# Kernel optimization log

Hardware: AMD Instinct MI355X
Metric: run time of the kernel (lower is better)

The kernel has to match this reference:

```python
import jax, jax.numpy as jnp
import numpy as np

B, LQ, LKV = 4, 2048, 2048
E, AUG, H = 2048, 1024, 16
DH = E // H
EPS = 1e-6


def setup_inputs() -> dict:
    key = jax.random.key(0)
    ks = jax.random.split(key, 6)
    s = lambda d: 1.0 / np.sqrt(d)
    return {
        "query": jax.random.normal(ks[0], (B, LQ, E), jnp.float32),
        "aug_hidden_state": jax.random.normal(ks[1], (B, LKV, AUG), jnp.float32),
        "aug_mask": jnp.ones((B, LKV), jnp.float32),
        "proj_w": jax.random.normal(ks[2], (E, AUG), jnp.float32) * s(AUG),
        "proj_b": jnp.zeros((E,), jnp.float32),
        "in_proj_w": jax.random.normal(ks[3], (3 * E, E), jnp.float32) * s(E),
        "in_proj_b": jnp.zeros((3 * E,), jnp.float32),
        "out_proj_w": jax.random.normal(ks[4], (E, E), jnp.float32) * s(E),
        "out_proj_b": jnp.zeros((E,), jnp.float32),
        "rms_w": jnp.zeros((E,), jnp.float32),
    }


def reference(query, aug_hidden_state, aug_mask, proj_w, proj_b,
              in_proj_w, in_proj_b, out_proj_w, out_proj_b, rms_w):
    del aug_mask  # asserted but never used by the original forward
    # key and value: two identical Linear calls in the original -> same tensor
    kv = aug_hidden_state @ proj_w.T + proj_b                      # [B,LKV,E]
    wq, wk, wv = jnp.split(in_proj_w, 3, axis=0)
    bq, bk, bv = jnp.split(in_proj_b, 3, axis=0)
    q = (query @ wq.T + bq).reshape(B, LQ, H, DH)
    k = (kv @ wk.T + bk).reshape(B, LKV, H, DH)
    v = (kv @ wv.T + bv).reshape(B, LKV, H, DH)
    scale = 1.0 / np.sqrt(DH)
    scores = jnp.einsum("bqhd,bkhd->bhqk", q * scale, k)           # [B,H,LQ,LKV]
    attn = jax.nn.softmax(scores, axis=-1)
    ctx = jnp.einsum("bhqk,bkhd->bqhd", attn, v).reshape(B, LQ, E)
    attn_out = ctx @ out_proj_w.T + out_proj_b                      # [B,LQ,E]
    # GemmaRMSNorm: fp32 norm, (1 + weight) gain
    x32 = attn_out.astype(jnp.float32)
    normed = x32 * jax.lax.rsqrt(jnp.mean(x32 * x32, axis=-1, keepdims=True) + EPS)
    attn_out = (normed * (1.0 + rms_w)).astype(attn_out.dtype)
    return attn_out + query
```

## Files before the change

kernel.cpp:

```cpp
#include <hip/hip_runtime.h>
#include <hip/hip_bf16.h>
#include <stdint.h>

#define B_   4
#define LQ_  2048
#define LKV_ 2048
#define E_   2048
#define AUG_ 1024
#define H_   16
#define DH_  128

typedef unsigned short u16;
typedef __bf16 bf16x8 __attribute__((ext_vector_type(8)));
typedef float f32x4 __attribute__((ext_vector_type(4)));
typedef float f32x16 __attribute__((ext_vector_type(16)));
typedef int i32x2 __attribute__((ext_vector_type(2)));

__device__ __forceinline__ u16 f2bf(float f) {
  union { float f; unsigned u; } v; v.f = f;
  unsigned r = v.u + 0x7fffu + ((v.u >> 16) & 1u);
  return (u16)(r >> 16);
}
__device__ __forceinline__ unsigned pk2(float a, float b) {
  return (unsigned)f2bf(a) | ((unsigned)f2bf(b) << 16);
}
__device__ __forceinline__ float bf2f(u16 u) {
  union { unsigned u; float f; } v; v.u = (unsigned)u << 16; return v.f;
}
__device__ __forceinline__ unsigned cvtpk_bf16(float lo, float hi) {
  unsigned r;
  asm("v_cvt_pk_bf16_f32 %0, %1, %2" : "=v"(r) : "v"(lo), "v"(hi));
  return r;
}
__device__ __forceinline__ float fast_ex2(float x) {
  float r;
  asm("v_exp_f32 %0, %1" : "=v"(r) : "v"(x));
  return r;
}

#define GLDS(gsrc, ldst)                                                        \
  __builtin_amdgcn_global_load_lds(                                             \
      (__attribute__((address_space(1))) void*)(uintptr_t)(gsrc),               \
      (__attribute__((address_space(3))) void*)(unsigned)(uintptr_t)(ldst),     \
      16, 0, 0)

#define BARRIER()                                   \
  do {                                              \
    asm volatile("" ::: "memory");                  \
    __builtin_amdgcn_s_barrier();                   \
    asm volatile("" ::: "memory");                  \
  } while (0)

__global__ __launch_bounds__(256) void cast5(const float* __restrict__ p0, u16* __restrict__ o0, int c0,
                                             const float* __restrict__ p1, u16* __restrict__ o1, int c1,
                                             const float* __restrict__ p2, u16* __restrict__ o2, int c2,
                                             const float* __restrict__ p3, u16* __restrict__ o3, int c3,
                                             const float* __restrict__ p4, u16* __restrict__ o4, int c4) {
  int stride = gridDim.x * blockDim.x;
  for (int i = blockIdx.x * blockDim.x + threadIdx.x; i < c4; i += stride) {
    const float* in; u16* out; int j;
    if (i < c0)      { in = p0; out = o0; j = i; }
    else if (i < c1) { in = p1; out = o1; j = i - c0; }
    else if (i < c2) { in = p2; out = o2; j = i - c1; }
    else if (i < c3) { in = p3; out = o3; j = i - c2; }
    else             { in = p4; out = o4; j = i - c3; }
    const float4* p = (const float4*)in + (size_t)j * 2;
    float4 a = p[0], b = p[1];
    uint4 o;
    o.x = pk2(a.x, a.y); o.y = pk2(a.z, a.w);
    o.z = pk2(b.x, b.y); o.w = pk2(b.z, b.w);
    ((uint4*)out)[j] = o;
  }
}

template <int OUTMODE>
__global__ __launch_bounds__(512, 2) void gemm_bt2(const u16* __restrict__ A,
                                                   const u16* __restrict__ W,
                                                   const float* __restrict__ bias,
                                                   void* __restrict__ Cp,
                                                   int N, int K) {
  __shared__ __align__(16) u16 As[3][256 * 32];
  __shared__ __align__(16) u16 Bs[3][256 * 32];
  const int tid = threadIdx.x;
  const int wave = tid >> 6, lane = tid & 63;
  const int wr = wave >> 2, wc = wave & 3;
  const int g = lane >> 4, r16 = lane & 15;
  const int m0 = blockIdx.y << 8, n0 = blockIdx.x << 8;

  size_t gA[2], gB[2];
  int ldst[2];
#pragma unroll
  for (int i = 0; i < 2; ++i) {
    int c = tid + i * 512;
    int s = c >> 6, w = c & 63;
    int wp = w ^ (((w >> 5) & 1) << 1);
    int grow = s * 16 + (wp >> 2);
    int gcol = (wp & 3) * 8;
    gA[i] = (size_t)(m0 + grow) * K + gcol;
    gB[i] = (size_t)(n0 + grow) * K + gcol;
    ldst[i] = c * 8;
  }
  const int aoff = r16 * 32 + ((g * 8) ^ ((r16 & 8) ? 16 : 0));

  f32x4 acc[8][4];
#pragma unroll
  for (int m = 0; m < 8; ++m)
#pragma unroll
    for (int n = 0; n < 4; ++n) acc[m][n] = (f32x4){0.f, 0.f, 0.f, 0.f};

  const int NT = K >> 5;
#pragma unroll
  for (int i = 0; i < 2; ++i) GLDS(A + gA[i], &As[0][ldst[i]]);
#pragma unroll
  for (int i = 0; i < 2; ++i) GLDS(W + gB[i], &Bs[0][ldst[i]]);
#pragma unroll
  for (int i = 0; i < 2; ++i) GLDS(A + gA[i] + 32, &As[1][ldst[i]]);
#pragma unroll
  for (int i = 0; i < 2; ++i) GLDS(W + gB[i] + 32, &Bs[1][ldst[i]]);

  int cur = 0;
  for (int t = 0; t < NT; ++t) {
    if (t + 1 < NT)
      asm volatile("s_waitcnt vmcnt(4)" ::: "memory");
    else
      asm volatile("s_waitcnt vmcnt(0)" ::: "memory");
    BARRIER();

    const u16* as = As[cur];
    const u16* bs = Bs[cur];
    int nxt = cur + 2; if (nxt >= 3) nxt -= 3;

    bf16x8 bfr[4], af[4];
#pragma unroll
    for (int n = 0; n < 4; ++n)
      bfr[n] = *(const bf16x8*)&bs[wc * 2048 + n * 512 + aoff];
#pragma unroll
    for (int m = 0; m < 4; ++m)
      af[m] = *(const bf16x8*)&as[wr * 4096 + m * 512 + aoff];
    if (t + 2 < NT) {
      size_t k0 = (size_t)(t + 2) * 32;
#pragma unroll
      for (int i = 0; i < 2; ++i) GLDS(A + gA[i] + k0, &As[nxt][ldst[i]]);
    }
    __builtin_amdgcn_s_setprio(1);
#pragma unroll
    for (int m = 0; m < 4; ++m)
#pragma unroll
      for (int n = 0; n < 4; ++n)
        acc[m][n] = __builtin_amdgcn_mfma_f32_16x16x32_bf16(af[m], bfr[n], acc[m][n], 0, 0, 0);
    __builtin_amdgcn_s_setprio(0);

    bf16x8 af2[4];
#pragma unroll
    for (int m = 0; m < 4; ++m)
      af2[m] = *(const bf16x8*)&as[wr * 4096 + (m + 4) * 512 + aoff];
    if (t + 2 < NT) {
      size_t k0 = (size_t)(t + 2) * 32;
#pragma unroll
      for (int i = 0; i < 2; ++i) GLDS(W + gB[i] + k0, &Bs[nxt][ldst[i]]);
    }
    __builtin_amdgcn_s_setprio(1);
#pragma unroll
    for (int m = 0; m < 4; ++m)
#pragma unroll
      for (int n = 0; n < 4; ++n)
        acc[m + 4][n] = __builtin_amdgcn_mfma_f32_16x16x32_bf16(af2[m], bfr[n], acc[m + 4][n], 0, 0, 0);
    __builtin_amdgcn_s_setprio(0);

    cur = cur + 1; if (cur >= 3) cur -= 3;
  }

  float bv[4];
#pragma unroll
  for (int n = 0; n < 4; ++n)
    bv[n] = bias ? bias[n0 + wc * 64 + n * 16 + r16] : 0.f;
#pragma unroll
  for (int m = 0; m < 8; ++m) {
    int row = m0 + wr * 128 + m * 16 + g * 4;
#pragma unroll
    for (int n = 0; n < 4; ++n) {
      int col = n0 + wc * 64 + n * 16 + r16;
      if (OUTMODE == 2) {
        size_t base = (((size_t)((row >> 11) * 16 + (col >> 7)) * 128 + (col & 127)) << 11) + (row & 2047);
        uint2 o2;
        o2.x = pk2(acc[m][n][0] + bv[n], acc[m][n][1] + bv[n]);
        o2.y = pk2(acc[m][n][2] + bv[n], acc[m][n][3] + bv[n]);
        *(uint2*)&((u16*)Cp)[base] = o2;
      } else {
#pragma unroll
        for (int r = 0; r < 4; ++r) {
          float v = acc[m][n][r] + bv[n];
          ((u16*)Cp)[(size_t)(row + r) * N + col] = f2bf(v);
        }
      }
    }
  }
}

__global__ __launch_bounds__(256) void transpose_w(const u16* __restrict__ in,
                                                   u16* __restrict__ out,
                                                   int R, int C) {
  __shared__ __align__(16) u16 t[64][72];
  int tid = threadIdx.x;
  int c0 = blockIdx.x << 6, r0 = blockIdx.y << 6;
  int gr = tid & 7, rw = tid >> 3;
#pragma unroll
  for (int p = 0; p < 2; ++p) {
    int row = rw + p * 32;
    uint4 x = *(const uint4*)&in[(size_t)(r0 + row) * C + c0 + gr * 8];
    *(uint4*)&t[row][gr * 8] = x;
  }
  __syncthreads();
#pragma unroll
  for (int p = 0; p < 2; ++p) {
    int d = rw + p * 32;
    u16 tmp[8];
#pragma unroll
    for (int j = 0; j < 8; ++j) tmp[j] = t[gr * 8 + j][d];
    uint4 o;
    o.x = (unsigned)tmp[0] | ((unsigned)tmp[1] << 16);
    o.y = (unsigned)tmp[2] | ((unsigned)tmp[3] << 16);
    o.z = (unsigned)tmp[4] | ((unsigned)tmp[5] << 16);
    o.w = (unsigned)tmp[6] | ((unsigned)tmp[7] << 16);
    *(uint4*)&out[(size_t)(c0 + d) * R + r0 + gr * 8] = o;
  }
}

__global__ __launch_bounds__(256) void gemv_bias(const u16* __restrict__ W,
                                                 const float* __restrict__ pb,
                                                 const float* __restrict__ base,
                                                 float* __restrict__ out, int K) {
  int row = blockIdx.x, tid = threadIdx.x;
  uint4 wv = ((const uint4*)(W + (size_t)row * K))[tid];
  const float4* pb4 = (const float4*)pb;
  float4 p0 = pb4[tid * 2], p1 = pb4[tid * 2 + 1];
  float s = bf2f((u16)(wv.x & 0xffff)) * p0.x + bf2f((u16)(wv.x >> 16)) * p0.y +
            bf2f((u16)(wv.y & 0xffff)) * p0.z + bf2f((u16)(wv.y >> 16)) * p0.w +
            bf2f((u16)(wv.z & 0xffff)) * p1.x + bf2f((u16)(wv.z >> 16)) * p1.y +
            bf2f((u16)(wv.w & 0xffff)) * p1.z + bf2f((u16)(wv.w >> 16)) * p1.w;
  s += __shfl_xor(s, 1);  s += __shfl_xor(s, 2);
  s += __shfl_xor(s, 4);  s += __shfl_xor(s, 8);
  s += __shfl_xor(s, 16); s += __shfl_xor(s, 32);
  __shared__ float ls[4];
  if ((tid & 63) == 0) ls[tid >> 6] = s;
  __syncthreads();
  if (tid == 0) out[row] = ls[0] + ls[1] + ls[2] + ls[3] + base[row];
}

__global__ __launch_bounds__(256) void attn_kernel(const u16* __restrict__ Q,
                                                   const u16* __restrict__ K,
                                                   const u16* __restrict__ Vt,
                                                   u16* __restrict__ Octx) {
  __shared__ __align__(16) u16 Ks[2][64 * 128];
  __shared__ __align__(16) u16 Vs[2][128 * 64];
  const int tid = threadIdx.x, wave = tid >> 6, lane = tid & 63;
  const int bid = blockIdx.x;
  const int qb = bid & 15, bh = bid >> 4, b = bh >> 4, h = bh & 15;
  const int q0 = qb << 7;
  const int l31 = lane & 31, hi = lane >> 5;
  const float Cs = 0.08838834764831845f * 1.4426950408889634f;

  const u16* Qp = Q + ((size_t)(b * LQ_ + q0 + wave * 32 + l31)) * E_ + h * DH_;
  const u16* Kp = K + ((size_t)(b * LKV_)) * E_ + h * DH_;
  const u16* Vp = Vt + (size_t)bh * DH_ * LKV_;

  const int kl_row = lane >> 4, kl_g = lane & 15;
  const int vl_row = lane >> 3, vl_g = lane & 7;

  bf16x8 qf[8];
#pragma unroll
  for (int c = 0; c < 8; ++c) {
    bf16x8 raw = *(const bf16x8*)&Qp[c * 16 + hi * 8];
#pragma unroll
    for (int j = 0; j < 8; ++j) qf[c][j] = (__bf16)((float)raw[j] * Cs);
  }

  bf16x8 VONES;
#pragma unroll
  for (int j = 0; j < 8; ++j) VONES[j] = (__bf16)1.0f;
  f32x16 FZERO = {};

  f32x16 o[4];
#pragma unroll
  for (int d = 0; d < 4; ++d)
#pragma unroll
    for (int r = 0; r < 16; ++r) o[d][r] = 0.f;
  f32x16 ol = {};

  auto STAGE = [&](int kv0, int buf) {
#pragma unroll
    for (int j = 0; j < 4; ++j) {
      int cc = wave * 4 + j;
      int krow = cc * 4 + kl_row;
      GLDS(Kp + (size_t)(kv0 + krow) * E_ + ((kl_g ^ (krow & 15)) << 3), &Ks[buf][cc * 512]);
      int vrow = cc * 8 + vl_row;
      GLDS(Vp + (size_t)vrow * LKV_ + kv0 + ((vl_g ^ (vrow & 7)) << 3), &Vs[buf][cc * 512]);
    }
  };

  const int NT = LKV_ / 64;
  STAGE(0, 0);

  for (int t = 0; t < NT; ++t) {
    const int cur = t & 1;
    if (t + 1 < NT) {
      STAGE((t + 1) * 64, cur ^ 1);
      asm volatile("s_waitcnt vmcnt(8)" ::: "memory");
    } else {
      asm volatile("s_waitcnt vmcnt(0)" ::: "memory");
    }
    BARRIER();

    const u16* ks = Ks[cur];
    const u16* vs = Vs[cur];

    f32x16 st[2];
#pragma unroll
    for (int n = 0; n < 2; ++n) {
      int row = n * 32 + l31;
      bf16x8 kf = *(const bf16x8*)&ks[row * 128 + ((hi ^ (row & 15)) << 3)];
      st[n] = __builtin_amdgcn_mfma_f32_32x32x16_bf16(kf, qf[0], FZERO, 0, 0, 0);
    }
#pragma unroll
    for (int c = 1; c < 8; ++c) {
#pragma unroll
      for (int n = 0; n < 2; ++n) {
        int row = n * 32 + l31;
        bf16x8 kf = *(const bf16x8*)&ks[row * 128 + (((c * 2 + hi) ^ (row & 15)) << 3)];
        st[n] = __builtin_amdgcn_mfma_f32_32x32x16_bf16(kf, qf[c], st[n], 0, 0, 0);
      }
    }

    unsigned AF[4][4];
#pragma unroll
    for (int n = 0; n < 2; ++n) {
      float pv[16];
#pragma unroll
      for (int r = 0; r < 16; ++r) pv[r] = fast_ex2(st[n][r]);
      unsigned a0 = cvtpk_bf16(pv[0], pv[1]),   a1 = cvtpk_bf16(pv[2], pv[3]);
      unsigned a2 = cvtpk_bf16(pv[4], pv[5]),   a3 = cvtpk_bf16(pv[6], pv[7]);
      unsigned b0 = cvtpk_bf16(pv[8], pv[9]),   b1 = cvtpk_bf16(pv[10], pv[11]);
      unsigned b2 = cvtpk_bf16(pv[12], pv[13]), b3 = cvtpk_bf16(pv[14], pv[15]);
      i32x2 r02 = __builtin_amdgcn_permlane32_swap((int)a0, (int)a2, false, false);
      i32x2 r13 = __builtin_amdgcn_permlane32_swap((int)a1, (int)a3, false, false);
      AF[n * 2][0] = (unsigned)r02[0]; AF[n * 2][1] = (unsigned)r13[0];
      AF[n * 2][2] = (unsigned)r02[1]; AF[n * 2][3] = (unsigned)r13[1];
      i32x2 s02 = __builtin_amdgcn_permlane32_swap((int)b0, (int)b2, false, false);
      i32x2 s13 = __builtin_amdgcn_permlane32_swap((int)b1, (int)b3, false, false);
      AF[n * 2 + 1][0] = (unsigned)s02[0]; AF[n * 2 + 1][1] = (unsigned)s13[0];
      AF[n * 2 + 1][2] = (unsigned)s02[1]; AF[n * 2 + 1][3] = (unsigned)s13[1];
    }

#pragma unroll
    for (int s = 0; s < 4; ++s) {
      union { unsigned u[4]; bf16x8 v; } pk;
      pk.u[0] = AF[s][0]; pk.u[1] = AF[s][1]; pk.u[2] = AF[s][2]; pk.u[3] = AF[s][3];
      bf16x8 pa = pk.v;
#pragma unroll
      for (int db = 0; db < 4; ++db) {
        int d = db * 32 + l31;
        bf16x8 vf = *(const bf16x8*)&vs[d * 64 + (((s * 2 + hi) ^ (d & 7)) << 3)];
        o[db] = __builtin_amdgcn_mfma_f32_32x32x16_bf16(pa, vf, o[db], 0, 0, 0);
      }
      ol = __builtin_amdgcn_mfma_f32_32x32x16_bf16(pa, VONES, ol, 0, 0, 0);
    }
    BARRIER();
  }

#pragma unroll
  for (int r = 0; r < 16; ++r) {
    int crow = (r & 3) + 8 * (r >> 2) + 4 * hi;
    float li = 1.0f / ol[r];
    size_t rb = ((size_t)(b * LQ_ + q0 + wave * 32 + crow)) * E_ + h * DH_ + l31;
#pragma unroll
    for (int db = 0; db < 4; ++db)
      Octx[rb + db * 32] = f2bf(o[db][r] * li);
  }
}

__global__ __launch_bounds__(256) void rms_res_bf(const u16* __restrict__ x,
                                                  const float* __restrict__ w,
                                                  const float* __restrict__ qres,
                                                  float* __restrict__ out) {
  int row = blockIdx.x, tid = threadIdx.x;
  uint4 xv = ((const uint4*)(x + (size_t)row * E_))[tid];
  float xf[8];
  xf[0] = bf2f((u16)(xv.x & 0xffff)); xf[1] = bf2f((u16)(xv.x >> 16));
  xf[2] = bf2f((u16)(xv.y & 0xffff)); xf[3] = bf2f((u16)(xv.y >> 16));
  xf[4] = bf2f((u16)(xv.z & 0xffff)); xf[5] = bf2f((u16)(xv.z >> 16));
  xf[6] = bf2f((u16)(xv.w & 0xffff)); xf[7] = bf2f((u16)(xv.w >> 16));
  float ss = 0.f;
#pragma unroll
  for (int j = 0; j < 8; ++j) ss += xf[j] * xf[j];
  ss += __shfl_xor(ss, 1);  ss += __shfl_xor(ss, 2);
  ss += __shfl_xor(ss, 4);  ss += __shfl_xor(ss, 8);
  ss += __shfl_xor(ss, 16); ss += __shfl_xor(ss, 32);
  __shared__ float ls[4];
  if ((tid & 63) == 0) ls[tid >> 6] = ss;
  __syncthreads();
  float total = ls[0] + ls[1] + ls[2] + ls[3];
  float rs = rsqrtf(total * (1.0f / (float)E_) + 1e-6f);
  const float4* qr = (const float4*)(qres + (size_t)row * E_);
  const float4* wr4 = (const float4*)w;
  float4 q0 = qr[tid * 2], q1 = qr[tid * 2 + 1];
  float4 w0 = wr4[tid * 2], w1 = wr4[tid * 2 + 1];
  float4 o0, o1;
  o0.x = xf[0] * rs * (1.f + w0.x) + q0.x;
  o0.y = xf[1] * rs * (1.f + w0.y) + q0.y;
  o0.z = xf[2] * rs * (1.f + w0.z) + q0.z;
  o0.w = xf[3] * rs * (1.f + w0.w) + q0.w;
  o1.x = xf[4] * rs * (1.f + w1.x) + q1.x;
  o1.y = xf[5] * rs * (1.f + w1.y) + q1.y;
  o1.z = xf[6] * rs * (1.f + w1.z) + q1.z;
  o1.w = xf[7] * rs * (1.f + w1.w) + q1.w;
  float4* op = (float4*)(out + (size_t)row * E_);
  op[tid * 2] = o0;
  op[tid * 2 + 1] = o1;
}

extern "C" void kernel_launch(void* const* d_in, const int* in_sizes, int n_in,
                              void* d_out, int out_size, void* d_ws, size_t ws_size,
                              hipStream_t stream) {
  const float* query = (const float*)d_in[0];
  const float* aug   = (const float*)d_in[1];
  const float* projw = (const float*)d_in[3];
  const float* projb = (const float*)d_in[4];
  const float* ipw   = (const float*)d_in[5];
  const float* ipb   = (const float*)d_in[6];
  const float* opw   = (const float*)d_in[7];
  const float* opb   = (const float*)d_in[8];
  const float* rmsw  = (const float*)d_in[9];

  char* ws = (char*)d_ws;
  size_t off = 0;
  auto alloc = [&](size_t bytes) {
    void* p = ws + off;
    off += (bytes + 1023) & ~(size_t)1023;
    return p;
  };
  u16* query_bf = (u16*)alloc((size_t)B_ * LQ_ * E_ * 2);
  u16* aug_bf   = (u16*)alloc((size_t)B_ * LKV_ * AUG_ * 2);
  u16* projw_bf = (u16*)alloc((size_t)E_ * AUG_ * 2);
  u16* w_bf     = (u16*)alloc((size_t)3 * E_ * E_ * 2);
  u16* outw_bf  = (u16*)alloc((size_t)E_ * E_ * 2);
  u16* kv_bf    = (u16*)alloc((size_t)B_ * LKV_ * E_ * 2);
  u16* q_bf     = (u16*)alloc((size_t)B_ * LQ_ * E_ * 2);
  u16* k_bf     = (u16*)alloc((size_t)B_ * LKV_ * E_ * 2);
  u16* v_bf     = (u16*)alloc((size_t)B_ * LKV_ * E_ * 2);
  u16* ctx_bf   = (u16*)alloc((size_t)B_ * LQ_ * E_ * 2);
  u16* attn_out = query_bf;
  u16* projwT = kv_bf;
  u16* wkv_f  = kv_bf + (size_t)AUG_ * E_;
  float* bkv  = (float*)(kv_bf + (size_t)AUG_ * E_ + (size_t)2 * E_ * AUG_);
  u16* vt_bf = v_bf;
  (void)in_sizes; (void)n_in; (void)ws_size;

  const int M = B_ * LQ_;

  const int n8_q  = (int)((size_t)M * E_ / 8);
  const int n8_a  = (int)((size_t)M * AUG_ / 8);
  const int n8_pw = (int)((size_t)E_ * AUG_ / 8);
  const int n8_iw = (int)((size_t)3 * E_ * E_ / 8);
  const int n8_ow = (int)((size_t)E_ * E_ / 8);
  const int cc0 = n8_q, cc1 = cc0 + n8_a, cc2 = cc1 + n8_pw, cc3 = cc2 + n8_iw,
            cc4 = cc3 + n8_ow;
  cast5<<<2048, 256, 0, stream>>>(query, query_bf, cc0,
                                  aug, aug_bf, cc1,
                                  projw, projw_bf, cc2,
                                  ipw, w_bf, cc3,
                                  opw, outw_bf, cc4);

  transpose_w<<<dim3(AUG_ / 64, E_ / 64), 256, 0, stream>>>(projw_bf, projwT, E_, AUG_);
  gemm_bt2<0><<<dim3(AUG_ / 256, (2 * E_) / 256), 512, 0, stream>>>(
      w_bf + (size_t)E_ * E_, projwT, nullptr, wkv_f, AUG_, E_);
  gemv_bias<<<2 * E_, 256, 0, stream>>>(w_bf + (size_t)E_ * E_, projb, ipb + E_, bkv, E_);

  gemm_bt2<0><<<dim3(E_ / 256, M / 256), 512, 0, stream>>>(query_bf, w_bf, ipb, q_bf, E_, E_);
  gemm_bt2<0><<<dim3(E_ / 256, M / 256), 512, 0, stream>>>(aug_bf, wkv_f, bkv, k_bf, E_, AUG_);
  gemm_bt2<2><<<dim3(E_ / 256, M / 256), 512, 0, stream>>>(
      aug_bf, wkv_f + (size_t)E_ * AUG_, bkv + E_, vt_bf, E_, AUG_);
  attn_kernel<<<B_ * H_ * (LQ_ / 128), 256, 0, stream>>>(q_bf, k_bf, vt_bf, ctx_bf);
  gemm_bt2<0><<<dim3(E_ / 256, M / 256), 512, 0, stream>>>(ctx_bf, outw_bf, opb, attn_out, E_, E_);
  rms_res_bf<<<M, 256, 0, stream>>>(attn_out, rmsw, query, (float*)d_out);
}
```

Baseline: 468.1 us.

## Switch GEMM to double-buffered 64-wide K tiles instead of triple-buffered 32

The bf16 GEMM loop now stages 64-wide K slices into two LDS buffers and prefetches the whole next slice right after the barrier. It no longer rotates through three 32-wide buffers with separately issued A and B loads. This halves the number of barriers and loop iterations per K sweep. In exchange, it raises LDS use to 128KB per block and waits on all outstanding loads (vmcnt(0)) every iteration. That leaves only one stage of prefetch depth to hide global-load latency.

```diff
diff --git a/kernel.cpp b/kernel.cpp
--- a/kernel.cpp
+++ b/kernel.cpp
@@ -79,8 +79,8 @@
                                                    const float* __restrict__ bias,
                                                    void* __restrict__ Cp,
                                                    int N, int K) {
-  __shared__ __align__(16) u16 As[3][256 * 32];
-  __shared__ __align__(16) u16 Bs[3][256 * 32];
+  __shared__ __align__(16) u16 As[2][256 * 64];
+  __shared__ __align__(16) u16 Bs[2][256 * 64];
   const int tid = threadIdx.x;
   const int wave = tid >> 6, lane = tid & 63;
   const int wr = wave >> 2, wc = wave & 3;
@@ -108,66 +108,59 @@
 #pragma unroll
     for (int n = 0; n < 4; ++n) acc[m][n] = (f32x4){0.f, 0.f, 0.f, 0.f};
 
-  const int NT = K >> 5;
-#pragma unroll
-  for (int i = 0; i < 2; ++i) GLDS(A + gA[i], &As[0][ldst[i]]);
-#pragma unroll
-  for (int i = 0; i < 2; ++i) GLDS(W + gB[i], &Bs[0][ldst[i]]);
-#pragma unroll
-  for (int i = 0; i < 2; ++i) GLDS(A + gA[i] + 32, &As[1][ldst[i]]);
-#pragma unroll
-  for (int i = 0; i < 2; ++i) GLDS(W + gB[i] + 32, &Bs[1][ldst[i]]);
-
+  const int NT = K >> 6;
+
+  auto STAGE = [&](int kt, int buf) {
+    size_t k0 = (size_t)kt * 64;
+#pragma unroll
+    for (int hh = 0; hh < 2; ++hh) {
+#pragma unroll
+      for (int i = 0; i < 2; ++i) {
+        GLDS(A + gA[i] + k0 + hh * 32, &As[buf][hh * 8192 + ldst[i]]);
+        GLDS(W + gB[i] + k0 + hh * 32, &Bs[buf][hh * 8192 + ldst[i]]);
+      }
+    }
+  };
+
+  STAGE(0, 0);
   int cur = 0;
   for (int t = 0; t < NT; ++t) {
-    if (t + 1 < NT)
-      asm volatile("s_waitcnt vmcnt(4)" ::: "memory");
-    else
-      asm volatile("s_waitcnt vmcnt(0)" ::: "memory");
+    asm volatile("s_waitcnt vmcnt(0)" ::: "memory");
     BARRIER();
-
-    const u16* as = As[cur];
-    const u16* bs = Bs[cur];
-    int nxt = cur + 2; if (nxt >= 3) nxt -= 3;
-
-    bf16x8 bfr[4], af[4];
-#pragma unroll
-    for (int n = 0; n < 4; ++n)
-      bfr[n] = *(const bf16x8*)&bs[wc * 2048 + n * 512 + aoff];
-#pragma unroll
-    for (int m = 0; m < 4; ++m)
-      af[m] = *(const bf16x8*)&as[wr * 4096 + m * 512 + aoff];
-    if (t + 2 < NT) {
-      size_t k0 = (size_t)(t + 2) * 32;
-#pragma unroll
-      for (int i = 0; i < 2; ++i) GLDS(A + gA[i] + k0, &As[nxt][ldst[i]]);
-    }
-    __builtin_amdgcn_s_setprio(1);
-#pragma unroll
-    for (int m = 0; m < 4; ++m)
+    if (t + 1 < NT) STAGE(t + 1, cur ^ 1);
+
+#pragma unroll
+    for (int hh = 0; hh < 2; ++hh) {
+      const u16* as = &As[cur][hh * 8192];
+      const u16* bs = &Bs[cur][hh * 8192];
+      bf16x8 bfr[4], af[4];
 #pragma unroll
       for (int n = 0; n < 4; ++n)
-        acc[m][n] = __builtin_amdgcn_mfma_f32_16x16x32_bf16(af[m], bfr[n], acc[m][n], 0, 0, 0);
-    __builtin_amdgcn_s_setprio(0);
-
-    bf16x8 af2[4];
-#pragma unroll
-    for (int m = 0; m < 4; ++m)
-      af2[m] = *(const bf16x8*)&as[wr * 4096 + (m + 4) * 512 + aoff];
-    if (t + 2 < NT) {
-      size_t k0 = (size_t)(t + 2) * 32;
-#pragma unroll
-      for (int i = 0; i < 2; ++i) GLDS(W + gB[i] + k0, &Bs[nxt][ldst[i]]);
-    }
-    __builtin_amdgcn_s_setprio(1);
-#pragma unroll
-    for (int m = 0; m < 4; ++m)
-#pragma unroll
-      for (int n = 0; n < 4; ++n)
-        acc[m + 4][n] = __builtin_amdgcn_mfma_f32_16x16x32_bf16(af2[m], bfr[n], acc[m + 4][n], 0, 0, 0);
-    __builtin_amdgcn_s_setprio(0);
-
-    cur = cur + 1; if (cur >= 3) cur -= 3;
+        bfr[n] = *(const bf16x8*)&bs[wc * 2048 + n * 512 + aoff];
+#pragma unroll
+      for (int m = 0; m < 4; ++m)
+        af[m] = *(const bf16x8*)&as[wr * 4096 + m * 512 + aoff];
+      __builtin_amdgcn_s_setprio(1);
+#pragma unroll
+      for (int m = 0; m < 4; ++m)
+#pragma unroll
+        for (int n = 0; n < 4; ++n)
+          acc[m][n] = __builtin_amdgcn_mfma_f32_16x16x32_bf16(af[m], bfr[n], acc[m][n], 0, 0, 0);
+      __builtin_amdgcn_s_setprio(0);
+
+      bf16x8 af2[4];
+#pragma unroll
+      for (int m = 0; m < 4; ++m)
+        af2[m] = *(const bf16x8*)&as[wr * 4096 + (m + 4) * 512 + aoff];
+      __builtin_amdgcn_s_setprio(1);
+#pragma unroll
+      for (int m = 0; m < 4; ++m)
+#pragma unroll
+        for (int n = 0; n < 4; ++n)
+          acc[m + 4][n] = __builtin_amdgcn_mfma_f32_16x16x32_bf16(af2[m], bfr[n], acc[m + 4][n], 0, 0, 0);
+      __builtin_amdgcn_s_setprio(0);
+    }
+    cur ^= 1;
   }
 
   float bv[4];
```

After: 494.2 us. 5.6% more time.
